# Kernel optimization log

Measured on AMD Instinct MI355X. Metric: run time of the kernel, lower is better.

The kernel has to match this reference:

```python
import jax, jax.numpy as jnp
import numpy as np

B, S, H, NH = 2, 2048, 1024, 16
D = H // NH
EPS = 1.1920929e-07  # torch fp32 finfo eps used by F.rms_norm default
ROPE_BASE = 10000.0


def setup_inputs() -> dict:
    key = jax.random.key(0)
    k0, k1, k2, k3 = jax.random.split(key, 4)
    return {
        "x": jax.random.normal(k0, (B, S, H), jnp.float32),
        "ve": jax.random.normal(k1, (B, S, H), jnp.float32),
        "W_qkv": jax.random.normal(k2, (3 * H, H), jnp.float32) * 0.02,
        "W_o": jax.random.normal(k3, (H, H), jnp.float32) * 0.02,
        "lambdas": jnp.array([0.5, 0.5], jnp.float32),
    }


def _rms_norm(x):
    # F.rms_norm without learnable weight, over last dim
    return x * jax.lax.rsqrt(jnp.mean(x * x, axis=-1, keepdims=True) + EPS)


def _rope(x):
    # x: [b, s, h, d]; rotate-half style RoPE matching the Rotary module
    d = x.shape[-1]
    inv_freq = (1.0 / ROPE_BASE) ** (jnp.arange(0, d, 2, dtype=jnp.float32) / d)
    t = jnp.arange(x.shape[1], dtype=jnp.float32)
    freqs = t[:, None] * inv_freq[None, :]          # [s, d/2]
    cos = jnp.cos(freqs)[None, :, None, :]
    sin = jnp.sin(freqs)[None, :, None, :]
    x1, x2 = jnp.split(x, 2, axis=-1)
    return jnp.concatenate([x1 * cos + x2 * sin, -x1 * sin + x2 * cos], axis=-1)


def reference(x, ve, W_qkv, W_o, lambdas):
    qkv = x @ W_qkv.T                                # [b, s, 3H]
    q, k, v = jnp.split(qkv, 3, axis=-1)
    rs = lambda a: a.reshape(B, S, NH, D)            # b s (h d) -> b s h d
    q, k, v = rs(q), rs(k), rs(v)
    q = _rope(_rms_norm(q))
    k = _rope(_rms_norm(k))
    v = lambdas[0] * v + lambdas[1] * rs(ve)         # value-lambda mix
    scale = 1.0 / jnp.sqrt(jnp.asarray(D, jnp.float32))  # flex_attention default
    scores = jnp.einsum('bqhd,bkhd->bhqk', q, k) * scale
    causal = jnp.tril(jnp.ones((S, S), bool))
    scores = jnp.where(causal[None, None], scores, jnp.asarray(-jnp.inf, scores.dtype))
    p = jax.nn.softmax(scores, axis=-1)
    a = jnp.einsum('bhqk,bkhd->bqhd', p, v).reshape(B, S, H)
    return a @ W_o.T
```

## Files before the change

kernel.cpp:

```cpp
#include <hip/hip_runtime.h>
#include <math.h>

typedef __bf16 bf16;
typedef __attribute__((ext_vector_type(8))) __bf16 bf16x8;
typedef __attribute__((ext_vector_type(4))) __bf16 bf16x4;
typedef __attribute__((ext_vector_type(4))) float f32x4;

#define B_  2
#define S_  2048
#define H_  1024
#define NH_ 16
#define D_  64

__device__ __forceinline__ f32x4 mfma16(bf16x8 a, bf16x8 b, f32x4 c) {
    return __builtin_amdgcn_mfma_f32_16x16x32_bf16(a, b, c, 0, 0, 0);
}

__device__ __forceinline__ void async16(void* lds, const void* g) {
    __builtin_amdgcn_global_load_lds(
        (const __attribute__((address_space(1))) unsigned int*)g,
        (__attribute__((address_space(3))) unsigned int*)lds, 16, 0, 0);
}

__global__ __launch_bounds__(256) void cvt_bf16(const float* __restrict__ src,
                                                bf16* __restrict__ dst, int n4) {
    int i = blockIdx.x * 256 + threadIdx.x;
    if (i >= n4) return;
    f32x4 v = *(const f32x4*)(src + (size_t)i * 4);
    bf16x4 o;
    o[0] = (bf16)v[0]; o[1] = (bf16)v[1]; o[2] = (bf16)v[2]; o[3] = (bf16)v[3];
    *(bf16x4*)(dst + (size_t)i * 4) = o;
}

template <int EPI>
__global__ __launch_bounds__(256) void gemm_bt(
    const bf16* __restrict__ A, const bf16* __restrict__ W,
    int M, int N, int K,
    float* __restrict__ outF,
    bf16* __restrict__ qb, bf16* __restrict__ kb, bf16* __restrict__ vtb,
    const float* __restrict__ ve, const float* __restrict__ lambdas)
{
    __shared__ bf16 Al[128][32];
    __shared__ bf16 Bl[128][32];
    const int m0   = blockIdx.y * 128;
    const int n0   = blockIdx.x * 128;
    const int tid  = threadIdx.x;
    const int lane = tid & 63;
    const int w    = tid >> 6;
    const int quad = lane >> 4;
    const int l16  = lane & 15;
    const int wm   = (w >> 1) * 64;
    const int wn   = (w & 1) * 64;
    const int arow = lane >> 2;
    const int achk = (lane & 3) ^ ((lane >> 2) & 3);

    const f32x4 Z4 = {0.f, 0.f, 0.f, 0.f};
    f32x4 acc[4][4];
#pragma unroll
    for (int i = 0; i < 4; ++i)
#pragma unroll
        for (int j = 0; j < 4; ++j) acc[i][j] = Z4;

    for (int k0 = 0; k0 < K; k0 += 32) {
        const bf16* gB = W + (size_t)(n0 + w * 32 + arow) * K + k0 + achk * 8;
        async16(&Bl[w * 32][0], gB);
        async16(&Bl[w * 32 + 16][0], gB + (size_t)16 * K);
        const bf16* gA = A + (size_t)(m0 + w * 32 + arow) * K + k0 + achk * 8;
        async16(&Al[w * 32][0], gA);
        async16(&Al[w * 32 + 16][0], gA + (size_t)16 * K);
        __syncthreads();
        bf16x8 af[4], bfg[4];
#pragma unroll
        for (int i = 0; i < 4; ++i)
            af[i]  = *(const bf16x8*)&Al[wm + i * 16 + l16][(quad ^ (l16 & 3)) * 8];
#pragma unroll
        for (int j = 0; j < 4; ++j)
            bfg[j] = *(const bf16x8*)&Bl[wn + j * 16 + l16][(quad ^ (l16 & 3)) * 8];
#pragma unroll
        for (int i = 0; i < 4; ++i)
#pragma unroll
            for (int j = 0; j < 4; ++j)
                acc[i][j] = mfma16(af[i], bfg[j], acc[i][j]);
        __syncthreads();
    }

    if constexpr (EPI == 1) {
#pragma unroll
        for (int i = 0; i < 4; ++i)
#pragma unroll
            for (int j = 0; j < 4; ++j)
#pragma unroll
                for (int r = 0; r < 4; ++r) {
                    int m = m0 + wm + i * 16 + quad * 4 + r;
                    int n = n0 + wn + j * 16 + l16;
                    outF[(size_t)m * N + n] = acc[i][j][r];
                }
    } else {
        const int nbase = n0 + wn;
        const int which = nbase >> 10;
        const int h     = (nbase & (H_ - 1)) >> 6;
        if (which < 2) {
            bf16* dst = which ? kb : qb;
            const float KF = -13.287712379549449f / 32.0f;
            const float fl = exp2f((float)l16 * KF);
            const float fh = exp2f((float)(l16 + 16) * KF);
#pragma unroll
            for (int i = 0; i < 4; ++i) {
                float ss[4];
#pragma unroll
                for (int r = 0; r < 4; ++r)
                    ss[r] = acc[i][0][r] * acc[i][0][r] + acc[i][1][r] * acc[i][1][r]
                          + acc[i][2][r] * acc[i][2][r] + acc[i][3][r] * acc[i][3][r];
#pragma unroll
                for (int r = 0; r < 4; ++r) {
                    ss[r] += __shfl_xor(ss[r], 1);
                    ss[r] += __shfl_xor(ss[r], 2);
                    ss[r] += __shfl_xor(ss[r], 4);
                    ss[r] += __shfl_xor(ss[r], 8);
                }
#pragma unroll
                for (int r = 0; r < 4; ++r) {
                    int   m   = m0 + wm + i * 16 + quad * 4 + r;
                    int   bb  = m >> 11, s = m & (S_ - 1);
                    float rms = rsqrtf(ss[r] * (1.0f / 64.0f) + 1.1920929e-07f);
                    float x0 = acc[i][0][r] * rms, x1 = acc[i][1][r] * rms;
                    float x2 = acc[i][2][r] * rms, x3 = acc[i][3][r] * rms;
                    float sl, cl, sh, ch;
                    sincosf((float)s * fl, &sl, &cl);
                    sincosf((float)s * fh, &sh, &ch);
                    bf16* bp = dst + ((size_t)(bb * NH_ + h) * S_ + s) * D_;
                    bp[l16]      = (bf16)(x0 * cl + x2 * sl);
                    bp[16 + l16] = (bf16)(x1 * ch + x3 * sh);
                    bp[32 + l16] = (bf16)(x2 * cl - x0 * sl);
                    bp[48 + l16] = (bf16)(x3 * ch - x1 * sh);
                }
            }
        } else {
            const float l0 = lambdas[0], l1 = lambdas[1];
#pragma unroll
            for (int i = 0; i < 4; ++i)
#pragma unroll
                for (int j = 0; j < 4; ++j)
#pragma unroll
                    for (int r = 0; r < 4; ++r) {
                        int   m  = m0 + wm + i * 16 + quad * 4 + r;
                        int   bb = m >> 11, s = m & (S_ - 1);
                        int   d  = j * 16 + l16;
                        float vm = l0 * acc[i][j][r]
                                 + l1 * ve[(size_t)m * H_ + h * 64 + d];
                        vtb[((size_t)(bb * NH_ + h) * D_ + d) * S_ + s] = (bf16)vm;
                    }
        }
    }
}

__global__ __launch_bounds__(256) void attn(
    const bf16* __restrict__ Q, const bf16* __restrict__ Kg,
    const bf16* __restrict__ Vt, bf16* __restrict__ Og)
{
    __shared__ bf16 Kl[2][64][64];
    __shared__ bf16 Vl[2][64][64];
    __shared__ bf16 Pl[4][16][64];

    const int bh   = blockIdx.y;
    const int b    = bh >> 4;
    const int h    = bh & 15;
    const int tid  = threadIdx.x;
    const int lane = tid & 63;
    const int w    = tid >> 6;
    const int quad = lane >> 4;
    const int l16  = lane & 15;
    const int l7   = l16 & 7;

    const bf16* Qp = Q  + (size_t)bh * S_ * D_;
    const bf16* Kp = Kg + (size_t)bh * S_ * D_;
    const bf16* Vp = Vt + (size_t)bh * D_ * S_;

    const int srow = lane >> 3;
    const int schk = (lane & 7) ^ (lane >> 3);
    const f32x4 Z4 = {0.f, 0.f, 0.f, 0.f};
    const float C1 = 0.18033688011112042f;
    const float C2 = -11.541560327111707f;

    auto stage = [&](int p, int kb0) {
        const bf16* gK = Kp + (size_t)(kb0 + w * 16 + srow) * D_ + schk * 8;
        async16(&Kl[p][w * 16][0], gK);
        async16(&Kl[p][w * 16 + 8][0], gK + (size_t)8 * D_);
        const bf16* gV = Vp + (size_t)(w * 16 + srow) * S_ + kb0 + schk * 8;
        async16(&Vl[p][w * 16][0], gV);
        async16(&Vl[p][w * 16 + 8][0], gV + (size_t)8 * S_);
    };

    for (int half = 0; half < 2; ++half) {
        const int qt    = half ? (31 - blockIdx.x) : blockIdx.x;
        const int qbase = qt * 64 + w * 16;
        const int qi    = qbase + l16;

        bf16x8 qf0 = *(const bf16x8*)(Qp + (size_t)(qbase + l16) * D_ + quad * 8);
        bf16x8 qf1 = *(const bf16x8*)(Qp + (size_t)(qbase + l16) * D_ + 32 + quad * 8);

        f32x4 of[4];
#pragma unroll
        for (int dt = 0; dt < 4; ++dt) of[dt] = Z4;
        float lsum = 0.f;

        const int nch = qt + 1;
        __syncthreads();
        stage(0, 0);
        for (int c = 0; c < nch; ++c) {
            const int p   = c & 1;
            const int kb0 = c * 64;
            __syncthreads();
            if (c + 1 < nch) stage(p ^ 1, kb0 + 64);

            float ps = 0.f;
#pragma unroll
            for (int nt = 0; nt < 4; ++nt) {
                bf16x8 kf0 = *(const bf16x8*)&Kl[p][nt * 16 + l16][(quad ^ l7) * 8];
                bf16x8 kf1 = *(const bf16x8*)&Kl[p][nt * 16 + l16][((quad + 4) ^ l7) * 8];
                f32x4 sacc = Z4;
                sacc = mfma16(kf0, qf0, sacc);
                sacc = mfma16(kf1, qf1, sacc);
                bf16x4 pk;
#pragma unroll
                for (int r = 0; r < 4; ++r) {
                    int   key = kb0 + nt * 16 + quad * 4 + r;
                    float e   = fmaf(sacc[r], C1, C2);
                    float pv  = (key <= qi) ? exp2f(e) : 0.f;
                    ps += pv;
                    pk[r] = (bf16)pv;
                }
                *(bf16x4*)&Pl[w][l16][((nt * 2 + (quad >> 1)) ^ l7) * 8 + (quad & 1) * 4] = pk;
            }
            ps += __shfl_xor(ps, 16);
            ps += __shfl_xor(ps, 32);
            lsum += ps;

            bf16x8 pf0 = *(const bf16x8*)&Pl[w][l16][(quad ^ l7) * 8];
            bf16x8 pf1 = *(const bf16x8*)&Pl[w][l16][((quad + 4) ^ l7) * 8];
#pragma unroll
            for (int dt = 0; dt < 4; ++dt) {
                bf16x8 vf0 = *(const bf16x8*)&Vl[p][dt * 16 + l16][(quad ^ l7) * 8];
                bf16x8 vf1 = *(const bf16x8*)&Vl[p][dt * 16 + l16][((quad + 4) ^ l7) * 8];
                of[dt] = mfma16(pf0, vf0, of[dt]);
                of[dt] = mfma16(pf1, vf1, of[dt]);
            }
        }

#pragma unroll
        for (int r = 0; r < 4; ++r) {
            float ld = __shfl(lsum, quad * 4 + r);
            float rl = 1.0f / ld;
            int   qq = qbase + quad * 4 + r;
#pragma unroll
            for (int dt = 0; dt < 4; ++dt)
                Og[((size_t)(b * S_ + qq)) * H_ + h * D_ + dt * 16 + l16] =
                    (bf16)(of[dt][r] * rl);
        }
    }
}

extern "C" void kernel_launch(void* const* d_in, const int* in_sizes, int n_in,
                              void* d_out, int out_size, void* d_ws, size_t ws_size,
                              hipStream_t stream)
{
    const float* x       = (const float*)d_in[0];
    const float* ve      = (const float*)d_in[1];
    const float* Wqkv    = (const float*)d_in[2];
    const float* Wo      = (const float*)d_in[3];
    const float* lambdas = (const float*)d_in[4];
    float* out = (float*)d_out;

    char* od = (char*)d_out;
    char* ws = (char*)d_ws;
    const size_t MB = 1024 * 1024;
    bf16* xb  = (bf16*)(od);
    bf16* wqb = (bf16*)(od + 8 * MB);
    bf16* qb  = (bf16*)(ws);
    bf16* kb  = (bf16*)(ws + 8 * MB);
    bf16* vtb = (bf16*)(ws + 16 * MB);
    bf16* ao  = (bf16*)(ws + 24 * MB);
    bf16* wob = (bf16*)(ws);

    cvt_bf16<<<4096, 256, 0, stream>>>(x, xb, (B_ * S_ * H_) / 4);
    cvt_bf16<<<3072, 256, 0, stream>>>(Wqkv, wqb, (3 * H_ * H_) / 4);
    gemm_bt<0><<<dim3(24, 32), 256, 0, stream>>>(
        xb, wqb, B_ * S_, 3 * H_, H_, nullptr, qb, kb, vtb, ve, lambdas);
    attn<<<dim3(16, B_ * NH_), 256, 0, stream>>>(qb, kb, vtb, ao);
    cvt_bf16<<<1024, 256, 0, stream>>>(Wo, wob, (H_ * H_) / 4);
    gemm_bt<1><<<dim3(8, 32), 256, 0, stream>>>(
        ao, wob, B_ * S_, H_, H_, out, nullptr, nullptr, nullptr, nullptr, nullptr);
}
```

Before: 244.1 us.

## Fuse conversions with RoPE table, vectorize V store, split attention grid, skip masking

The two fp32-to-bf16 conversion launches are merged into one kernel, which also precomputes a cos/sin RoPE table that the QKV GEMM epilogue reads instead of calling sincosf per element. The V-transpose store now packs four bf16 values per write. Attention drops the paired-half loop and uses one block per query tile, launched longest-first, and it evaluates the causal mask only on the diagonal chunk. Together these cut launch count, transcendental work and per-element mask checks, at the cost of extra table memory traffic and an imbalanced grid with more blocks.

```diff
diff --git a/kernel.cpp b/kernel.cpp
--- a/kernel.cpp
+++ b/kernel.cpp
@@ -22,13 +22,37 @@
         (__attribute__((address_space(3))) unsigned int*)lds, 16, 0, 0);
 }
 
+__global__ __launch_bounds__(256) void cvt_main(
+    const float* __restrict__ x, const float* __restrict__ wqkv,
+    bf16* __restrict__ xb, bf16* __restrict__ wqb, float2* __restrict__ tab)
+{
+    const int bid = blockIdx.x, tid = threadIdx.x;
+    if (bid < 4096) {
+        int i = bid * 256 + tid;
+        f32x4 v = *(const f32x4*)(x + (size_t)i * 4);
+        bf16x4 o; o[0]=(bf16)v[0]; o[1]=(bf16)v[1]; o[2]=(bf16)v[2]; o[3]=(bf16)v[3];
+        *(bf16x4*)(xb + (size_t)i * 4) = o;
+    } else if (bid < 7168) {
+        int i = (bid - 4096) * 256 + tid;
+        f32x4 v = *(const f32x4*)(wqkv + (size_t)i * 4);
+        bf16x4 o; o[0]=(bf16)v[0]; o[1]=(bf16)v[1]; o[2]=(bf16)v[2]; o[3]=(bf16)v[3];
+        *(bf16x4*)(wqb + (size_t)i * 4) = o;
+    } else {
+        int idx = (bid - 7168) * 256 + tid;
+        int s = idx >> 5, i = idx & 31;
+        float f = exp2f((float)i * (-13.287712379549449f / 32.0f));
+        float sn, cs;
+        sincosf((float)s * f, &sn, &cs);
+        tab[idx] = make_float2(cs, sn);
+    }
+}
+
 __global__ __launch_bounds__(256) void cvt_bf16(const float* __restrict__ src,
                                                 bf16* __restrict__ dst, int n4) {
     int i = blockIdx.x * 256 + threadIdx.x;
     if (i >= n4) return;
     f32x4 v = *(const f32x4*)(src + (size_t)i * 4);
-    bf16x4 o;
-    o[0] = (bf16)v[0]; o[1] = (bf16)v[1]; o[2] = (bf16)v[2]; o[3] = (bf16)v[3];
+    bf16x4 o; o[0]=(bf16)v[0]; o[1]=(bf16)v[1]; o[2]=(bf16)v[2]; o[3]=(bf16)v[3];
     *(bf16x4*)(dst + (size_t)i * 4) = o;
 }
 
@@ -38,7 +62,8 @@
     int M, int N, int K,
     float* __restrict__ outF,
     bf16* __restrict__ qb, bf16* __restrict__ kb, bf16* __restrict__ vtb,
-    const float* __restrict__ ve, const float* __restrict__ lambdas)
+    const float* __restrict__ ve, const float* __restrict__ lambdas,
+    const float2* __restrict__ tab)
 {
     __shared__ bf16 Al[128][32];
     __shared__ bf16 Bl[128][32];
@@ -101,9 +126,6 @@
         const int h     = (nbase & (H_ - 1)) >> 6;
         if (which < 2) {
             bf16* dst = which ? kb : qb;
-            const float KF = -13.287712379549449f / 32.0f;
-            const float fl = exp2f((float)l16 * KF);
-            const float fh = exp2f((float)(l16 + 16) * KF);
 #pragma unroll
             for (int i = 0; i < 4; ++i) {
                 float ss[4];
@@ -120,36 +142,39 @@
                 }
 #pragma unroll
                 for (int r = 0; r < 4; ++r) {
-                    int   m   = m0 + wm + i * 16 + quad * 4 + r;
-                    int   bb  = m >> 11, s = m & (S_ - 1);
-                    float rms = rsqrtf(ss[r] * (1.0f / 64.0f) + 1.1920929e-07f);
-                    float x0 = acc[i][0][r] * rms, x1 = acc[i][1][r] * rms;
-                    float x2 = acc[i][2][r] * rms, x3 = acc[i][3][r] * rms;
-                    float sl, cl, sh, ch;
-                    sincosf((float)s * fl, &sl, &cl);
-                    sincosf((float)s * fh, &sh, &ch);
-                    bf16* bp = dst + ((size_t)(bb * NH_ + h) * S_ + s) * D_;
-                    bp[l16]      = (bf16)(x0 * cl + x2 * sl);
-                    bp[16 + l16] = (bf16)(x1 * ch + x3 * sh);
-                    bp[32 + l16] = (bf16)(x2 * cl - x0 * sl);
-                    bp[48 + l16] = (bf16)(x3 * ch - x1 * sh);
+                    int    m   = m0 + wm + i * 16 + quad * 4 + r;
+                    int    bb  = m >> 11, s = m & (S_ - 1);
+                    float  rms = rsqrtf(ss[r] * (1.0f / 64.0f) + 1.1920929e-07f);
+                    float  x0 = acc[i][0][r] * rms, x1 = acc[i][1][r] * rms;
+                    float  x2 = acc[i][2][r] * rms, x3 = acc[i][3][r] * rms;
+                    float2 t0 = tab[(size_t)s * 32 + l16];
+                    float2 t1 = tab[(size_t)s * 32 + 16 + l16];
+                    bf16*  bp = dst + ((size_t)(bb * NH_ + h) * S_ + s) * D_;
+                    bp[l16]      = (bf16)(x0 * t0.x + x2 * t0.y);
+                    bp[16 + l16] = (bf16)(x1 * t1.x + x3 * t1.y);
+                    bp[32 + l16] = (bf16)(x2 * t0.x - x0 * t0.y);
+                    bp[48 + l16] = (bf16)(x3 * t1.x - x1 * t1.y);
                 }
             }
         } else {
             const float l0 = lambdas[0], l1 = lambdas[1];
 #pragma unroll
-            for (int i = 0; i < 4; ++i)
-#pragma unroll
-                for (int j = 0; j < 4; ++j)
+            for (int i = 0; i < 4; ++i) {
+                const int m00 = m0 + wm + i * 16 + quad * 4;
+                const int bb  = m00 >> 11, s = m00 & (S_ - 1);
+#pragma unroll
+                for (int j = 0; j < 4; ++j) {
+                    const int d = j * 16 + l16;
+                    bf16x4 pk;
 #pragma unroll
                     for (int r = 0; r < 4; ++r) {
-                        int   m  = m0 + wm + i * 16 + quad * 4 + r;
-                        int   bb = m >> 11, s = m & (S_ - 1);
-                        int   d  = j * 16 + l16;
                         float vm = l0 * acc[i][j][r]
-                                 + l1 * ve[(size_t)m * H_ + h * 64 + d];
-                        vtb[((size_t)(bb * NH_ + h) * D_ + d) * S_ + s] = (bf16)vm;
+                                 + l1 * ve[(size_t)(m00 + r) * H_ + h * 64 + d];
+                        pk[r] = (bf16)vm;
                     }
+                    *(bf16x4*)&vtb[((size_t)(bb * NH_ + h) * D_ + d) * S_ + s] = pk;
+                }
+            }
         }
     }
 }
@@ -165,6 +190,7 @@
     const int bh   = blockIdx.y;
     const int b    = bh >> 4;
     const int h    = bh & 15;
+    const int qt   = gridDim.x - 1 - blockIdx.x;
     const int tid  = threadIdx.x;
     const int lane = tid & 63;
     const int w    = tid >> 6;
@@ -181,6 +207,17 @@
     const f32x4 Z4 = {0.f, 0.f, 0.f, 0.f};
     const float C1 = 0.18033688011112042f;
     const float C2 = -11.541560327111707f;
+
+    const int qbase = qt * 64 + w * 16;
+    const int qi    = qbase + l16;
+
+    bf16x8 qf0 = *(const bf16x8*)(Qp + (size_t)(qbase + l16) * D_ + quad * 8);
+    bf16x8 qf1 = *(const bf16x8*)(Qp + (size_t)(qbase + l16) * D_ + 32 + quad * 8);
+
+    f32x4 of[4];
+#pragma unroll
+    for (int dt = 0; dt < 4; ++dt) of[dt] = Z4;
+    float lsum = 0.f;
 
     auto stage = [&](int p, int kb0) {
         const bf16* gK = Kp + (size_t)(kb0 + w * 16 + srow) * D_ + schk * 8;
@@ -191,29 +228,16 @@
         async16(&Vl[p][w * 16 + 8][0], gV + (size_t)8 * S_);
     };
 
-    for (int half = 0; half < 2; ++half) {
-        const int qt    = half ? (31 - blockIdx.x) : blockIdx.x;
-        const int qbase = qt * 64 + w * 16;
-        const int qi    = qbase + l16;
-
-        bf16x8 qf0 = *(const bf16x8*)(Qp + (size_t)(qbase + l16) * D_ + quad * 8);
-        bf16x8 qf1 = *(const bf16x8*)(Qp + (size_t)(qbase + l16) * D_ + 32 + quad * 8);
-
-        f32x4 of[4];
-#pragma unroll
-        for (int dt = 0; dt < 4; ++dt) of[dt] = Z4;
-        float lsum = 0.f;
-
-        const int nch = qt + 1;
+    stage(0, 0);
+    const int nch = qt + 1;
+    for (int c = 0; c < nch; ++c) {
+        const int p   = c & 1;
+        const int kb0 = c * 64;
         __syncthreads();
-        stage(0, 0);
-        for (int c = 0; c < nch; ++c) {
-            const int p   = c & 1;
-            const int kb0 = c * 64;
-            __syncthreads();
-            if (c + 1 < nch) stage(p ^ 1, kb0 + 64);
-
-            float ps = 0.f;
+        if (c + 1 < nch) stage(p ^ 1, kb0 + 64);
+
+        float ps = 0.f;
+        if (c < qt) {
 #pragma unroll
             for (int nt = 0; nt < 4; ++nt) {
                 bf16x8 kf0 = *(const bf16x8*)&Kl[p][nt * 16 + l16][(quad ^ l7) * 8];
@@ -224,39 +248,55 @@
                 bf16x4 pk;
 #pragma unroll
                 for (int r = 0; r < 4; ++r) {
-                    int   key = kb0 + nt * 16 + quad * 4 + r;
-                    float e   = fmaf(sacc[r], C1, C2);
-                    float pv  = (key <= qi) ? exp2f(e) : 0.f;
+                    float pv = exp2f(fmaf(sacc[r], C1, C2));
                     ps += pv;
                     pk[r] = (bf16)pv;
                 }
                 *(bf16x4*)&Pl[w][l16][((nt * 2 + (quad >> 1)) ^ l7) * 8 + (quad & 1) * 4] = pk;
             }
-            ps += __shfl_xor(ps, 16);
-            ps += __shfl_xor(ps, 32);
-            lsum += ps;
-
-            bf16x8 pf0 = *(const bf16x8*)&Pl[w][l16][(quad ^ l7) * 8];
-            bf16x8 pf1 = *(const bf16x8*)&Pl[w][l16][((quad + 4) ^ l7) * 8];
-#pragma unroll
-            for (int dt = 0; dt < 4; ++dt) {
-                bf16x8 vf0 = *(const bf16x8*)&Vl[p][dt * 16 + l16][(quad ^ l7) * 8];
-                bf16x8 vf1 = *(const bf16x8*)&Vl[p][dt * 16 + l16][((quad + 4) ^ l7) * 8];
-                of[dt] = mfma16(pf0, vf0, of[dt]);
-                of[dt] = mfma16(pf1, vf1, of[dt]);
+        } else {
+#pragma unroll
+            for (int nt = 0; nt < 4; ++nt) {
+                bf16x8 kf0 = *(const bf16x8*)&Kl[p][nt * 16 + l16][(quad ^ l7) * 8];
+                bf16x8 kf1 = *(const bf16x8*)&Kl[p][nt * 16 + l16][((quad + 4) ^ l7) * 8];
+                f32x4 sacc = Z4;
+                sacc = mfma16(kf0, qf0, sacc);
+                sacc = mfma16(kf1, qf1, sacc);
+                bf16x4 pk;
+#pragma unroll
+                for (int r = 0; r < 4; ++r) {
+                    int   key = kb0 + nt * 16 + quad * 4 + r;
+                    float pv  = (key <= qi) ? exp2f(fmaf(sacc[r], C1, C2)) : 0.f;
+                    ps += pv;
+                    pk[r] = (bf16)pv;
+                }
+                *(bf16x4*)&Pl[w][l16][((nt * 2 + (quad >> 1)) ^ l7) * 8 + (quad & 1) * 4] = pk;
             }
         }
-
-#pragma unroll
-        for (int r = 0; r < 4; ++r) {
-            float ld = __shfl(lsum, quad * 4 + r);
-            float rl = 1.0f / ld;
-            int   qq = qbase + quad * 4 + r;
-#pragma unroll
-            for (int dt = 0; dt < 4; ++dt)
-                Og[((size_t)(b * S_ + qq)) * H_ + h * D_ + dt * 16 + l16] =
-                    (bf16)(of[dt][r] * rl);
+        ps += __shfl_xor(ps, 16);
+        ps += __shfl_xor(ps, 32);
+        lsum += ps;
+
+        bf16x8 pf0 = *(const bf16x8*)&Pl[w][l16][(quad ^ l7) * 8];
+        bf16x8 pf1 = *(const bf16x8*)&Pl[w][l16][((quad + 4) ^ l7) * 8];
+#pragma unroll
+        for (int dt = 0; dt < 4; ++dt) {
+            bf16x8 vf0 = *(const bf16x8*)&Vl[p][dt * 16 + l16][(quad ^ l7) * 8];
+            bf16x8 vf1 = *(const bf16x8*)&Vl[p][dt * 16 + l16][((quad + 4) ^ l7) * 8];
+            of[dt] = mfma16(pf0, vf0, of[dt]);
+            of[dt] = mfma16(pf1, vf1, of[dt]);
         }
+    }
+
+#pragma unroll
+    for (int r = 0; r < 4; ++r) {
+        float ld = __shfl(lsum, quad * 4 + r);
+        float rl = 1.0f / ld;
+        int   qq = qbase + quad * 4 + r;
+#pragma unroll
+        for (int dt = 0; dt < 4; ++dt)
+            Og[((size_t)(b * S_ + qq)) * H_ + h * D_ + dt * 16 + l16] =
+                (bf16)(of[dt][r] * rl);
     }
 }
 
@@ -274,20 +314,20 @@
     char* od = (char*)d_out;
     char* ws = (char*)d_ws;
     const size_t MB = 1024 * 1024;
-    bf16* xb  = (bf16*)(od);
-    bf16* wqb = (bf16*)(od + 8 * MB);
-    bf16* qb  = (bf16*)(ws);
-    bf16* kb  = (bf16*)(ws + 8 * MB);
-    bf16* vtb = (bf16*)(ws + 16 * MB);
-    bf16* ao  = (bf16*)(ws + 24 * MB);
-    bf16* wob = (bf16*)(ws);
-
-    cvt_bf16<<<4096, 256, 0, stream>>>(x, xb, (B_ * S_ * H_) / 4);
-    cvt_bf16<<<3072, 256, 0, stream>>>(Wqkv, wqb, (3 * H_ * H_) / 4);
+    bf16*   xb  = (bf16*)(od);
+    bf16*   wqb = (bf16*)(od + 8 * MB);
+    float2* tab = (float2*)(od + 14 * MB);
+    bf16*   qb  = (bf16*)(ws);
+    bf16*   kb  = (bf16*)(ws + 8 * MB);
+    bf16*   vtb = (bf16*)(ws + 16 * MB);
+    bf16*   ao  = (bf16*)(ws + 24 * MB);
+    bf16*   wob = (bf16*)(ws);
+
+    cvt_main<<<7424, 256, 0, stream>>>(x, Wqkv, xb, wqb, tab);
     gemm_bt<0><<<dim3(24, 32), 256, 0, stream>>>(
-        xb, wqb, B_ * S_, 3 * H_, H_, nullptr, qb, kb, vtb, ve, lambdas);
-    attn<<<dim3(16, B_ * NH_), 256, 0, stream>>>(qb, kb, vtb, ao);
+        xb, wqb, B_ * S_, 3 * H_, H_, nullptr, qb, kb, vtb, ve, lambdas, (const float2*)tab);
+    attn<<<dim3(32, B_ * NH_), 256, 0, stream>>>(qb, kb, vtb, ao);
     cvt_bf16<<<1024, 256, 0, stream>>>(Wo, wob, (H_ * H_) / 4);
     gemm_bt<1><<<dim3(8, 32), 256, 0, stream>>>(
-        ao, wob, B_ * S_, H_, H_, out, nullptr, nullptr, nullptr, nullptr, nullptr);
-}
+        ao, wob, B_ * S_, H_, H_, out, nullptr, nullptr, nullptr, nullptr, nullptr, nullptr);
+}
```

Measured after the change: 245.0 us. About the same (+0.4%).
